# Kernel optimization log

Hardware: AMD Instinct MI355X
Metric: run time of the kernel (lower is better)

The kernel has to match this reference:

```python
import jax, jax.numpy as jnp
import numpy as np

B, N, Q, D, H = 8, 2048, 256, 1024, 16
HD = D // H


def setup_inputs() -> dict:
    key = jax.random.key(0)
    ks = jax.random.split(key, 6)
    scale = 1.0 / np.sqrt(D)
    return {
        "sources": jax.random.normal(ks[0], (B, N, D), dtype=jnp.float32),
        "queries": jax.random.normal(ks[1], (B, Q, D), dtype=jnp.float32),
        "w_in": jax.random.normal(ks[2], (3 * D, D), dtype=jnp.float32) * scale,
        "b_in": jax.random.normal(ks[3], (3 * D,), dtype=jnp.float32) * 0.02,
        "w_out": jax.random.normal(ks[4], (D, D), dtype=jnp.float32) * scale,
        "b_out": jax.random.normal(ks[5], (D,), dtype=jnp.float32) * 0.02,
    }


def reference(sources, queries, w_in, b_in, w_out, b_out):
    # torch nn.MultiheadAttention (batch_first, eval mode, no attn_mask),
    # applied per-sample with equal lengths == one batched cross-attention.
    w_q, w_k, w_v = jnp.split(w_in, 3, axis=0)   # each [D, D]
    b_q, b_k, b_v = jnp.split(b_in, 3, axis=0)
    q = queries @ w_q.T + b_q                    # [B, Q, D]
    k = sources @ w_k.T + b_k                    # [B, N, D]
    v = sources @ w_v.T + b_v                    # [B, N, D]
    q = q.reshape(B, Q, H, HD)
    k = k.reshape(B, N, H, HD)
    v = v.reshape(B, N, H, HD)
    scale = 1.0 / np.sqrt(HD).astype(np.float32)
    scores = jnp.einsum("bqhd,bkhd->bhqk", q, k) * scale  # [B, H, Q, N]
    attn = jax.nn.softmax(scores, axis=-1)
    out = jnp.einsum("bhqk,bkhd->bqhd", attn, v).reshape(B, Q, D)
    out = out @ w_out.T + b_out                  # out_proj
    return out + queries                         # residual (fix=False: no norm)
```

## Files before the change

### kernel.cpp

```cpp
#include <hip/hip_runtime.h>
#include <hip/hip_bf16.h>


typedef unsigned short u16;
typedef __attribute__((ext_vector_type(8))) short short8;
typedef __attribute__((ext_vector_type(4))) float floatx4;

static_assert(sizeof(short8) == 16, "short8 must be 16B");

__device__ __forceinline__ u16 f2bf(float f) {
  unsigned int x = __float_as_uint(f);
  x += 0x7fffu + ((x >> 16) & 1u);
  return (u16)(x >> 16);
}

__device__ __forceinline__ float bf2f(u16 b) {
  return __uint_as_float(((unsigned int)b) << 16);
}

__device__ __forceinline__ void gload16(const u16* g, u16* lds) {
  __builtin_amdgcn_global_load_lds(
      (const __attribute__((address_space(1))) unsigned int*)g,
      (__attribute__((address_space(3))) unsigned int*)lds, 16, 0, 0);
}

template <int N> __device__ __forceinline__ void vmwait() {
  if constexpr (N == 0)      asm volatile("s_waitcnt vmcnt(0)" ::: "memory");
  else if constexpr (N == 4) asm volatile("s_waitcnt vmcnt(4)" ::: "memory");
  else if constexpr (N == 6) asm volatile("s_waitcnt vmcnt(6)" ::: "memory");
  else if constexpr (N == 8) asm volatile("s_waitcnt vmcnt(8)" ::: "memory");
  else static_assert(N == 0, "unsupported vmcnt immediate");
}

__device__ __forceinline__ void lgkm0() {
  asm volatile("s_waitcnt lgkmcnt(0)" ::: "memory");
}

__device__ __forceinline__ void sfence() { __builtin_amdgcn_sched_barrier(0); }

__global__ __launch_bounds__(256) void f2bf_multi(
    const float* __restrict__ s, u16* __restrict__ so,
    const float* __restrict__ q, u16* __restrict__ qo,
    const float* __restrict__ wi, u16* __restrict__ wio,
    const float* __restrict__ wo, u16* __restrict__ woo) {
  int i = blockIdx.x * 256 + threadIdx.x;
  const float* in; u16* out; int idx;
  if (i < 4194304)      { in = s;  out = so;  idx = i; }
  else if (i < 4718592) { in = q;  out = qo;  idx = i - 4194304; }
  else if (i < 5505024) { in = wi; out = wio; idx = i - 4718592; }
  else if (i < 5767168) { in = wo; out = woo; idx = i - 5505024; }
  else return;
  float4 v = reinterpret_cast<const float4*>(in)[idx];
  ushort4 o;
  o.x = f2bf(v.x); o.y = f2bf(v.y); o.z = f2bf(v.z); o.w = f2bf(v.w);
  reinterpret_cast<ushort4*>(out)[idx] = o;
}

template <int MT, int NT>
__device__ __forceinline__ void gemm_core(
    const u16* __restrict__ A, int lda,
    const u16* __restrict__ Bm, int ldb, int K,
    u16* __restrict__ Alds, u16* __restrict__ Blds,
    floatx4 (&acc)[MT][NT]) {
  const int t = threadIdx.x;
  const int wave = t >> 6, lane = t & 63;
  const int rr = lane & 15, kq = lane >> 4;
  constexpr int AI = MT, BI = NT;
  constexpr int AELEMS = MT * 32 * 64;
  constexpr int BELEMS = NT * 32 * 64;

  const u16* ag[AI]; u16* al[AI];
#pragma unroll
  for (int i = 0; i < AI; ++i) {
    int s = i * 256 + t;
    int row = s >> 3, c16 = s & 7;
    ag[i] = A + (size_t)row * lda + ((c16 ^ (row & 7)) * 8);
    al[i] = Alds + (size_t)(i * 256 + wave * 64) * 8;
  }
  const u16* bg[BI]; u16* blp[BI];
#pragma unroll
  for (int i = 0; i < BI; ++i) {
    int s = i * 256 + t;
    int row = s >> 3, c16 = s & 7;
    bg[i] = Bm + (size_t)row * ldb + ((c16 ^ (row & 7)) * 8);
    blp[i] = Blds + (size_t)(i * 256 + wave * 64) * 8;
  }

  const int m0w = (wave & 1) * (MT * 16);
  const int n0w = (wave >> 1) * (NT * 16);
  int aoff[MT][2], boff[NT][2];
#pragma unroll
  for (int mi = 0; mi < MT; ++mi) {
    int row = m0w + mi * 16 + rr;
#pragma unroll
    for (int kk = 0; kk < 2; ++kk)
      aoff[mi][kk] = row * 64 + (((kk * 4 + kq) ^ (row & 7)) * 8);
  }
#pragma unroll
  for (int ni = 0; ni < NT; ++ni) {
    int row = n0w + ni * 16 + rr;
#pragma unroll
    for (int kk = 0; kk < 2; ++kk)
      boff[ni][kk] = row * 64 + (((kk * 4 + kq) ^ (row & 7)) * 8);
  }

  auto compute = [&](int bs) {
    const u16* Ab = Alds + bs * AELEMS;
    const u16* Bb = Blds + bs * BELEMS;
#pragma unroll
    for (int kk = 0; kk < 2; ++kk) {
      short8 af[MT], bfr[NT];
#pragma unroll
      for (int mi = 0; mi < MT; ++mi)
        af[mi] = *reinterpret_cast<const short8*>(Ab + aoff[mi][kk]);
#pragma unroll
      for (int ni = 0; ni < NT; ++ni)
        bfr[ni] = *reinterpret_cast<const short8*>(Bb + boff[ni][kk]);
      __builtin_amdgcn_s_setprio(1);
#pragma unroll
      for (int mi = 0; mi < MT; ++mi)
#pragma unroll
        for (int ni = 0; ni < NT; ++ni)
          acc[mi][ni] = __builtin_amdgcn_mfma_f32_16x16x32_bf16(af[mi], bfr[ni], acc[mi][ni], 0, 0, 0);
      __builtin_amdgcn_s_setprio(0);
    }
  };

  const int nt = K >> 6;

#pragma unroll
  for (int i = 0; i < AI; ++i) gload16(ag[i], al[i]);
#pragma unroll
  for (int i = 0; i < BI; ++i) gload16(bg[i], blp[i]);

  int cur = 0;
#pragma unroll 1
  for (int tt = 0; tt < nt - 1; ++tt) {
    const int nxt = cur ^ 1;
    const int koff = (tt + 1) * 64;
#pragma unroll
    for (int i = 0; i < AI; ++i) gload16(ag[i] + koff, al[i] + nxt * AELEMS);
#pragma unroll
    for (int i = 0; i < BI; ++i) gload16(bg[i] + koff, blp[i] + nxt * BELEMS);
    sfence();
    vmwait<AI + BI>();
    __builtin_amdgcn_s_barrier();
    sfence();
    compute(cur);
    sfence();
    __builtin_amdgcn_s_barrier();
    cur = nxt;
  }
  sfence();
  vmwait<0>();
  __builtin_amdgcn_s_barrier();
  sfence();
  compute(cur);
}

template <int LO>
__device__ __forceinline__ void read_a8(const u16* ab, int kcol0, int kcol1,
                                        short8 (&af)[8][2]) {
#pragma unroll
  for (int mi = 0; mi < 4; ++mi) {
    af[LO + mi][0] = *reinterpret_cast<const short8*>(ab + (LO + mi) * 1024 + kcol0);
    af[LO + mi][1] = *reinterpret_cast<const short8*>(ab + (LO + mi) * 1024 + kcol1);
  }
}

template <int LO>
__device__ __forceinline__ void read_b8(const u16* bb, int kcol0, int kcol1,
                                        short8 (&bf)[4][2]) {
#pragma unroll
  for (int ni = 0; ni < 2; ++ni) {
    bf[LO + ni][0] = *reinterpret_cast<const short8*>(bb + (LO + ni) * 1024 + kcol0);
    bf[LO + ni][1] = *reinterpret_cast<const short8*>(bb + (LO + ni) * 1024 + kcol1);
  }
}

template <int M0, int N0>
__device__ __forceinline__ void quad8(const short8 (&af)[8][2], const short8 (&bf)[4][2],
                                      floatx4 (&acc)[8][4]) {
  __builtin_amdgcn_s_setprio(1);
#pragma unroll
  for (int kk = 0; kk < 2; ++kk)
#pragma unroll
    for (int mi = 0; mi < 4; ++mi)
#pragma unroll
      for (int ni = 0; ni < 2; ++ni)
        acc[M0 + mi][N0 + ni] = __builtin_amdgcn_mfma_f32_16x16x32_bf16(
            af[M0 + mi][kk], bf[N0 + ni][kk], acc[M0 + mi][N0 + ni], 0, 0, 0);
  __builtin_amdgcn_s_setprio(0);
}

__global__ __launch_bounds__(512, 2) void gemm_proj_kv8(
    const u16* __restrict__ s_bf, const u16* __restrict__ wi_bf,
    const float* __restrict__ b_in,
    u16* __restrict__ kp, u16* __restrict__ vT) {
  __shared__ __attribute__((aligned(16))) u16 Alds[2 * 256 * 64];
  __shared__ __attribute__((aligned(16))) u16 Blds[2 * 256 * 64];

  int bid = blockIdx.y * 8 + blockIdx.x;
  int nb = (bid & 7) * 64 + (bid >> 3);
  const int by = nb >> 3, bx = nb & 7;
  const int mB = by * 256;
  const int nB = bx * 256;
  const u16* Ag = s_bf + (size_t)mB * 1024;
  const u16* Wg = wi_bf + (size_t)(1024 + nB) * 1024;
  const float* bias = b_in + 1024 + nB;

  const int t = threadIdx.x;
  const int w = t >> 6, lane = t & 63;
  const int rr = lane & 15, kq = lane >> 4;
  const int wr = w >> 2, wc = w & 3;

  const u16* ga[2][2]; const u16* gb[2][2];
#pragma unroll
  for (int h = 0; h < 2; ++h)
#pragma unroll
    for (int i = 0; i < 2; ++i) {
      int s = i * 512 + t;
      int row = h * 128 + (s >> 3), c16 = s & 7;
      ga[h][i] = Ag + (size_t)row * 1024 + ((c16 ^ (row & 7)) * 8);
      gb[h][i] = Wg + (size_t)row * 1024 + ((c16 ^ (row & 7)) * 8);
    }

#define STAGE_A8(j, h) { const int d_ = ((j) & 1) * 16384;                         \
    gload16(ga[h][0] + (size_t)(j) * 64, Alds + d_ + (h) * 8192 + w * 512);        \
    gload16(ga[h][1] + (size_t)(j) * 64, Alds + d_ + (h) * 8192 + 4096 + w * 512); }
#define STAGE_B8(j, h) { const int d_ = ((j) & 1) * 16384;                         \
    gload16(gb[h][0] + (size_t)(j) * 64, Blds + d_ + (h) * 8192 + w * 512);        \
    gload16(gb[h][1] + (size_t)(j) * 64, Blds + d_ + (h) * 8192 + 4096 + w * 512); }

  const int kcol0 = ((kq) ^ (rr & 7)) * 8;
  const int kcol1 = ((4 + kq) ^ (rr & 7)) * 8;
  const u16* abase = Alds + (wr * 128 + rr) * 64;
  const u16* bbase = Blds + (wc * 64 + rr) * 64;

  short8 af[8][2], bf[4][2];
  const floatx4 zz = {0.f, 0.f, 0.f, 0.f};
  floatx4 acc[8][4];
#pragma unroll
  for (int mi = 0; mi < 8; ++mi)
#pragma unroll
    for (int ni = 0; ni < 4; ++ni) acc[mi][ni] = zz;

  STAGE_A8(0, 0); STAGE_B8(0, 0); STAGE_A8(0, 1); STAGE_B8(0, 1);
  STAGE_A8(1, 0); STAGE_B8(1, 0);
  sfence();
  vmwait<4>();
  __builtin_amdgcn_s_barrier();
  sfence();

#pragma unroll 1
  for (int kt = 0; kt < 16; ++kt) {
    const int doff = (kt & 1) * 16384;
    const u16* ab = abase + doff;
    const u16* bb = bbase + doff;
    read_a8<0>(ab, kcol0, kcol1, af);
    read_b8<0>(bb, kcol0, kcol1, bf);
    if (kt + 1 < 16) STAGE_A8(kt + 1, 1);
    sfence();
    __builtin_amdgcn_s_barrier();
    lgkm0(); sfence();
    quad8<0, 0>(af, bf, acc);
    sfence();
    __builtin_amdgcn_s_barrier();
    sfence();
    read_a8<4>(ab, kcol0, kcol1, af);
    read_b8<2>(bb, kcol0, kcol1, bf);
    if (kt + 1 < 16) STAGE_B8(kt + 1, 1);
    sfence();
    __builtin_amdgcn_s_barrier();
    lgkm0(); sfence();
    quad8<0, 2>(af, bf, acc);
    sfence();
    __builtin_amdgcn_s_barrier();
    sfence();
    if (kt + 2 < 16) STAGE_A8(kt + 2, 0);
    sfence();
    __builtin_amdgcn_s_barrier();
    quad8<4, 0>(af, bf, acc);
    sfence();
    __builtin_amdgcn_s_barrier();
    sfence();
    if (kt + 2 < 16) { STAGE_B8(kt + 2, 0); sfence(); vmwait<4>(); }
    else             { sfence(); vmwait<0>(); }
    __builtin_amdgcn_s_barrier();
    quad8<4, 2>(af, bf, acc);
    sfence();
    __builtin_amdgcn_s_barrier();
    sfence();
  }
#undef STAGE_A8
#undef STAGE_B8

  const int r4 = kq * 4;
  const int m0w = wr * 128, n0w = wc * 64;
  if (nB < 1024) {
#pragma unroll
    for (int mi = 0; mi < 8; ++mi)
#pragma unroll
      for (int ni = 0; ni < 4; ++ni) {
        int nl = n0w + ni * 16 + rr;
        float bv = bias[nl];
#pragma unroll
        for (int r = 0; r < 4; ++r) {
          int m = mB + m0w + mi * 16 + r4 + r;
          kp[(size_t)m * 1024 + nB + nl] = f2bf(acc[mi][ni][r] + bv);
        }
      }
  } else {
#pragma unroll
    for (int mi = 0; mi < 8; ++mi)
#pragma unroll
      for (int ni = 0; ni < 4; ++ni) {
        int n2 = nB + n0w + ni * 16 + rr - 1024;
        int h = n2 >> 6, d = n2 & 63;
        float bv = bias[n0w + ni * 16 + rr];
        int m0 = mB + m0w + mi * 16 + r4;
        int b = m0 >> 11, j0 = m0 & 2047;
        ushort4 o;
        o.x = f2bf(acc[mi][ni][0] + bv);
        o.y = f2bf(acc[mi][ni][1] + bv);
        o.z = f2bf(acc[mi][ni][2] + bv);
        o.w = f2bf(acc[mi][ni][3] + bv);
        *reinterpret_cast<ushort4*>(
            vT + ((size_t)(b * 16 + h) * 64 + d) * 2048 + j0) = o;
      }
  }
}

__global__ __launch_bounds__(256, 2) void gemm_proj_q(
    const u16* __restrict__ qy_bf, const u16* __restrict__ wi_bf,
    const float* __restrict__ b_in, u16* __restrict__ qp) {
  __shared__ __attribute__((aligned(16))) u16 Alds[2 * 128 * 64];
  __shared__ __attribute__((aligned(16))) u16 Blds[2 * 128 * 64];
  const int mB = blockIdx.y * 128;
  const int nB = blockIdx.x * 128;
  const u16* A = qy_bf + (size_t)mB * 1024;
  const u16* W = wi_bf + (size_t)nB * 1024;
  const float* bias = b_in + nB;

  const floatx4 zz = {0.f, 0.f, 0.f, 0.f};
  floatx4 acc[4][4] = {{zz, zz, zz, zz}, {zz, zz, zz, zz}, {zz, zz, zz, zz}, {zz, zz, zz, zz}};
  gemm_core<4, 4>(A, 1024, W, 1024, 1024, Alds, Blds, acc);

  const int lane = threadIdx.x & 63, wave = threadIdx.x >> 6;
  const int rr = lane & 15, r4 = (lane >> 4) * 4;
  const int m0w = (wave & 1) * 64, n0w = (wave >> 1) * 64;
#pragma unroll
  for (int mi = 0; mi < 4; ++mi)
#pragma unroll
    for (int ni = 0; ni < 4; ++ni) {
      int nl = n0w + ni * 16 + rr;
      float bv = bias[nl];
#pragma unroll
      for (int r = 0; r < 4; ++r) {
        int m = mB + m0w + mi * 16 + r4 + r;
        qp[(size_t)m * 1024 + nB + nl] = f2bf((acc[mi][ni][r] + bv) * 0.125f);
      }
    }
}

__global__ __launch_bounds__(512, 2) void attn_fused(
    const u16* __restrict__ qp, const u16* __restrict__ kp,
    const u16* __restrict__ vT, u16* __restrict__ ao) {
  __shared__ __attribute__((aligned(16))) u16 Qlds[8192];
  __shared__ __attribute__((aligned(16))) u16 Klds[2][8192];
  __shared__ __attribute__((aligned(16))) u16 Vlds[2][8192];
  __shared__ __attribute__((aligned(16))) u16 Plds[16384];
  __shared__ float l_part[4][128];

  const int bid = blockIdx.x;
  const int nb = (bid & 7) * 32 + (bid >> 3);
  const int bh = nb >> 1, qh = nb & 1;
  const int b = bh >> 4, h = bh & 15;

  const int t = threadIdx.x;
  const int w = t >> 6, lane = t & 63;
  const int rr = lane & 15, kq = lane >> 4;
  const int swz = rr & 7;
  const int wrS = w >> 2, wcS = w & 3;
  const int wrP = w >> 1, wcP = w & 1;

  const u16* qg[2]; const u16* kg[2]; const u16* vg[2];
  {
    const u16* qbase = qp + ((size_t)(b * 256 + qh * 128)) * 1024 + h * 64;
    const u16* kbase = kp + ((size_t)b * 2048) * 1024 + h * 64;
    const u16* vbase = vT + ((size_t)bh * 64) * 2048;
#pragma unroll
    for (int i = 0; i < 2; ++i) {
      int s = i * 512 + t;
      int r8 = s >> 3, c8 = s & 7;
      int r16 = s >> 4, c16 = s & 15;
      qg[i] = qbase + (size_t)r8 * 1024 + ((c8 ^ (r8 & 7)) * 8);
      kg[i] = kbase + (size_t)r8 * 1024 + ((c8 ^ (r8 & 7)) * 8);
      vg[i] = vbase + (size_t)r16 * 2048 + ((c16 ^ (r16 & 7)) * 8);
    }
  }

  float l_acc[4][4];
#pragma unroll
  for (int mi = 0; mi < 4; ++mi)
#pragma unroll
    for (int r = 0; r < 4; ++r) l_acc[mi][r] = 0.f;
  const floatx4 zz = {0.f, 0.f, 0.f, 0.f};
  floatx4 oacc[2][2] = {{zz, zz}, {zz, zz}};

  ((float*)l_part)[t] = 0.f;
#pragma unroll
  for (int i = 0; i < 2; ++i) gload16(qg[i], Qlds + (i * 512 + w * 64) * 8);
#pragma unroll
  for (int i = 0; i < 2; ++i) gload16(kg[i], &Klds[0][(i * 512 + w * 64) * 8]);
#pragma unroll
  for (int i = 0; i < 2; ++i) gload16(vg[i], &Vlds[0][(i * 512 + w * 64) * 8]);
  sfence();
  vmwait<0>();
  __builtin_amdgcn_s_barrier();
  sfence();

  short8 qf[4][2];
#pragma unroll
  for (int mi = 0; mi < 4; ++mi) {
    int qrow = wrS * 64 + mi * 16 + rr;
#pragma unroll
    for (int kc = 0; kc < 2; ++kc)
      qf[mi][kc] = *reinterpret_cast<const short8*>(
          Qlds + qrow * 64 + (((kc * 4 + kq) ^ swz) * 8));
  }

#pragma unroll 1
  for (int kt = 0; kt < 16; ++kt) {
    const int buf = kt & 1;
    if (kt) { sfence(); __builtin_amdgcn_s_barrier(); sfence(); }
    if (kt < 15) {
      const int nxt = buf ^ 1;
      const size_t ko = (size_t)(kt + 1) * 131072;
      const size_t vo = (size_t)(kt + 1) * 128;
#pragma unroll
      for (int i = 0; i < 2; ++i) gload16(kg[i] + ko, &Klds[nxt][(i * 512 + w * 64) * 8]);
#pragma unroll
      for (int i = 0; i < 2; ++i) gload16(vg[i] + vo, &Vlds[nxt][(i * 512 + w * 64) * 8]);
      sfence();
      vmwait<4>();
    } else {
      sfence();
      vmwait<0>();
    }
    short8 kf[2][2];
#pragma unroll
    for (int ni = 0; ni < 2; ++ni) {
      int krow = wcS * 32 + ni * 16 + rr;
#pragma unroll
      for (int kc = 0; kc < 2; ++kc)
        kf[ni][kc] = *reinterpret_cast<const short8*>(
            &Klds[buf][krow * 64 + (((kc * 4 + kq) ^ swz) * 8)]);
    }
    lgkm0(); sfence();
    floatx4 sacc[4][2];
#pragma unroll
    for (int mi = 0; mi < 4; ++mi)
#pragma unroll
      for (int ni = 0; ni < 2; ++ni) sacc[mi][ni] = zz;
    __builtin_amdgcn_s_setprio(1);
#pragma unroll
    for (int kc = 0; kc < 2; ++kc)
#pragma unroll
      for (int mi = 0; mi < 4; ++mi)
#pragma unroll
        for (int ni = 0; ni < 2; ++ni)
          sacc[mi][ni] = __builtin_amdgcn_mfma_f32_16x16x32_bf16(
              qf[mi][kc], kf[ni][kc], sacc[mi][ni], 0, 0, 0);
    __builtin_amdgcn_s_setprio(0);
    sfence();
#pragma unroll
    for (int mi = 0; mi < 4; ++mi) {
#pragma unroll
      for (int r = 0; r < 4; ++r) {
        int qr = wrS * 64 + mi * 16 + kq * 4 + r;
        int rb = qr * 128;
        int qsw = qr & 7;
        float lsum = 0.f;
#pragma unroll
        for (int ni = 0; ni < 2; ++ni) {
          int key = wcS * 32 + ni * 16 + rr;
          u16 pb = f2bf(__expf(sacc[mi][ni][r]));
          Plds[rb + ((((key >> 3) ^ qsw)) << 3) + (key & 7)] = pb;
          lsum += bf2f(pb);
        }
        l_acc[mi][r] += lsum;
      }
    }
    lgkm0();
    sfence();
    __builtin_amdgcn_s_barrier();
    sfence();
    short8 pa[2][4], vf[2][4];
#pragma unroll
    for (int mi = 0; mi < 2; ++mi) {
      int qrow = wrP * 32 + mi * 16 + rr;
#pragma unroll
      for (int kc = 0; kc < 4; ++kc)
        pa[mi][kc] = *reinterpret_cast<const short8*>(
            Plds + qrow * 128 + ((((kc * 4 + kq) ^ swz)) << 3));
    }
#pragma unroll
    for (int ni = 0; ni < 2; ++ni) {
      int drow = wcP * 32 + ni * 16 + rr;
#pragma unroll
      for (int kc = 0; kc < 4; ++kc)
        vf[ni][kc] = *reinterpret_cast<const short8*>(
            &Vlds[buf][drow * 128 + ((((kc * 4 + kq) ^ swz)) << 3)]);
    }
    lgkm0(); sfence();
    __builtin_amdgcn_s_setprio(1);
#pragma unroll
    for (int kc = 0; kc < 4; ++kc)
#pragma unroll
      for (int mi = 0; mi < 2; ++mi)
#pragma unroll
        for (int ni = 0; ni < 2; ++ni)
          oacc[mi][ni] = __builtin_amdgcn_mfma_f32_16x16x32_bf16(
              pa[mi][kc], vf[ni][kc], oacc[mi][ni], 0, 0, 0);
    __builtin_amdgcn_s_setprio(0);
    sfence();
  }

#pragma unroll
  for (int mi = 0; mi < 4; ++mi)
#pragma unroll
    for (int r = 0; r < 4; ++r) {
      float v = l_acc[mi][r];
      v += __shfl_xor(v, 1, 64);
      v += __shfl_xor(v, 2, 64);
      v += __shfl_xor(v, 4, 64);
      v += __shfl_xor(v, 8, 64);
      l_acc[mi][r] = v;
    }
  if (rr == 0) {
#pragma unroll
    for (int mi = 0; mi < 4; ++mi)
#pragma unroll
      for (int r = 0; r < 4; ++r)
        l_part[wcS][wrS * 64 + mi * 16 + kq * 4 + r] = l_acc[mi][r];
  }
  __syncthreads();

  u16* aob = ao + ((size_t)(b * 256 + qh * 128)) * 1024 + h * 64;
#pragma unroll
  for (int mi = 0; mi < 2; ++mi)
#pragma unroll
    for (int r = 0; r < 4; ++r) {
      int q = wrP * 32 + mi * 16 + kq * 4 + r;
      float inv = 1.0f / (l_part[0][q] + l_part[1][q] + l_part[2][q] + l_part[3][q]);
#pragma unroll
      for (int ni = 0; ni < 2; ++ni) {
        int d = wcP * 32 + ni * 16 + rr;
        aob[(size_t)q * 1024 + d] = f2bf(oacc[mi][ni][r] * inv);
      }
    }
}

__global__ __launch_bounds__(256, 2) void gemm_out(
    const u16* __restrict__ A, const u16* __restrict__ W,
    const float* __restrict__ bias, const float* __restrict__ resid,
    float* __restrict__ out) {
  __shared__ __attribute__((aligned(16))) u16 Alds[2 * 64 * 64];
  __shared__ __attribute__((aligned(16))) u16 Blds[2 * 128 * 64];
  const int mB = blockIdx.y * 64;
  const int nB = blockIdx.x * 128;
  const floatx4 zz = {0.f, 0.f, 0.f, 0.f};
  floatx4 acc[2][4] = {{zz, zz, zz, zz}, {zz, zz, zz, zz}};
  gemm_core<2, 4>(A + (size_t)mB * 1024, 1024, W + (size_t)nB * 1024, 1024, 1024,
                  Alds, Blds, acc);
  const int lane = threadIdx.x & 63, wave = threadIdx.x >> 6;
  const int rr = lane & 15, r4 = (lane >> 4) * 4;
  const int m0w = (wave & 1) * 32, n0w = (wave >> 1) * 64;
#pragma unroll
  for (int mi = 0; mi < 2; ++mi)
#pragma unroll
    for (int ni = 0; ni < 4; ++ni) {
      int n = nB + n0w + ni * 16 + rr;
      float bv = bias[n];
#pragma unroll
      for (int r = 0; r < 4; ++r) {
        int m = mB + m0w + mi * 16 + r4 + r;
        size_t idx = (size_t)m * 1024 + n;
        out[idx] = acc[mi][ni][r] + bv + resid[idx];
      }
    }
}

extern "C" void kernel_launch(void* const* d_in, const int* in_sizes, int n_in,
                              void* d_out, int out_size, void* d_ws, size_t ws_size,
                              hipStream_t stream) {
  const float* sources = (const float*)d_in[0];
  const float* queries = (const float*)d_in[1];
  const float* w_in    = (const float*)d_in[2];
  const float* b_in    = (const float*)d_in[3];
  const float* w_out   = (const float*)d_in[4];
  const float* b_out   = (const float*)d_in[5];
  float* out = (float*)d_out;

  char* ws = (char*)d_ws;
  size_t off = 0;
  auto alloc = [&](size_t elems) -> u16* {
    u16* p = (u16*)(ws + off);
    off += elems * sizeof(u16);
    off = (off + 255) & ~(size_t)255;
    return p;
  };
  u16* s_bf  = alloc((size_t)16777216);
  u16* qy_bf = alloc((size_t)2097152);
  u16* wi_bf = alloc((size_t)3145728);
  u16* wo_bf = alloc((size_t)1048576);
  u16* qp    = alloc((size_t)2097152);
  u16* kp    = alloc((size_t)16777216);
  u16* vT    = alloc((size_t)16777216);
  u16* ao    = alloc((size_t)2097152);

  f2bf_multi<<<dim3(22528), 256, 0, stream>>>(
      sources, s_bf, queries, qy_bf, w_in, wi_bf, w_out, wo_bf);

  gemm_proj_kv8<<<dim3(8, 64), 512, 0, stream>>>(s_bf, wi_bf, b_in, kp, vT);
  gemm_proj_q<<<dim3(8, 16), 256, 0, stream>>>(qy_bf, wi_bf, b_in, qp);

  attn_fused<<<dim3(256), 512, 0, stream>>>(qp, kp, vT, ao);

  gemm_out<<<dim3(8, 32), 256, 0, stream>>>(ao, wo_bf, b_out, queries, out);
}
```

Measured before the change: 275.8 us.

## Restructure attention kernel into 64-query blocks with MFMA row-sum and staggered K/V prefetch

```diff
diff --git a/kernel.cpp b/kernel.cpp
--- a/kernel.cpp
+++ b/kernel.cpp
@@ -14,8 +14,10 @@
   return (u16)(x >> 16);
 }
 
-__device__ __forceinline__ float bf2f(u16 b) {
-  return __uint_as_float(((unsigned int)b) << 16);
+__device__ __forceinline__ unsigned int cvtpk(float lo, float hi) {
+  unsigned int r;
+  asm("v_cvt_pk_bf16_f32 %0, %1, %2" : "=v"(r) : "v"(lo), "v"(hi));
+  return r;
 }
 
 __device__ __forceinline__ void gload16(const u16* g, u16* lds) {
@@ -26,6 +28,7 @@
 
 template <int N> __device__ __forceinline__ void vmwait() {
   if constexpr (N == 0)      asm volatile("s_waitcnt vmcnt(0)" ::: "memory");
+  else if constexpr (N == 2) asm volatile("s_waitcnt vmcnt(2)" ::: "memory");
   else if constexpr (N == 4) asm volatile("s_waitcnt vmcnt(4)" ::: "memory");
   else if constexpr (N == 6) asm volatile("s_waitcnt vmcnt(6)" ::: "memory");
   else if constexpr (N == 8) asm volatile("s_waitcnt vmcnt(8)" ::: "memory");
@@ -363,202 +366,178 @@
     }
 }
 
-__global__ __launch_bounds__(512, 2) void attn_fused(
+__global__ __launch_bounds__(512, 4) void attn_fused(
     const u16* __restrict__ qp, const u16* __restrict__ kp,
     const u16* __restrict__ vT, u16* __restrict__ ao) {
-  __shared__ __attribute__((aligned(16))) u16 Qlds[8192];
   __shared__ __attribute__((aligned(16))) u16 Klds[2][8192];
   __shared__ __attribute__((aligned(16))) u16 Vlds[2][8192];
-  __shared__ __attribute__((aligned(16))) u16 Plds[16384];
-  __shared__ float l_part[4][128];
+  __shared__ __attribute__((aligned(16))) u16 Plds[8192];
 
   const int bid = blockIdx.x;
-  const int nb = (bid & 7) * 32 + (bid >> 3);
-  const int bh = nb >> 1, qh = nb & 1;
+  const int nb = (bid & 7) * 64 + (bid >> 3);
+  const int bh = nb >> 2, qb = nb & 3;
   const int b = bh >> 4, h = bh & 15;
 
   const int t = threadIdx.x;
   const int w = t >> 6, lane = t & 63;
   const int rr = lane & 15, kq = lane >> 4;
-  const int swz = rr & 7;
-  const int wrS = w >> 2, wcS = w & 3;
-  const int wrP = w >> 1, wcP = w & 1;
-
-  const u16* qg[2]; const u16* kg[2]; const u16* vg[2];
+  const int wk = w >> 1, wq = w & 1;
+  const int wPq = w >> 2, wPd = w & 3;
+
+  const u16* qg;
+  const u16* kg[2];
+  const u16* vg[2];
   {
-    const u16* qbase = qp + ((size_t)(b * 256 + qh * 128)) * 1024 + h * 64;
+    const u16* qbase = qp + ((size_t)(b * 256 + qb * 64)) * 1024 + h * 64;
     const u16* kbase = kp + ((size_t)b * 2048) * 1024 + h * 64;
     const u16* vbase = vT + ((size_t)bh * 64) * 2048;
+    { int row = t >> 3, c8 = t & 7;
+      qg = qbase + (size_t)row * 1024 + ((c8 ^ (row & 7)) * 8); }
 #pragma unroll
     for (int i = 0; i < 2; ++i) {
       int s = i * 512 + t;
       int r8 = s >> 3, c8 = s & 7;
       int r16 = s >> 4, c16 = s & 15;
-      qg[i] = qbase + (size_t)r8 * 1024 + ((c8 ^ (r8 & 7)) * 8);
       kg[i] = kbase + (size_t)r8 * 1024 + ((c8 ^ (r8 & 7)) * 8);
       vg[i] = vbase + (size_t)r16 * 2048 + ((c16 ^ (r16 & 7)) * 8);
     }
   }
 
-  float l_acc[4][4];
-#pragma unroll
-  for (int mi = 0; mi < 4; ++mi)
-#pragma unroll
-    for (int r = 0; r < 4; ++r) l_acc[mi][r] = 0.f;
-  const floatx4 zz = {0.f, 0.f, 0.f, 0.f};
-  floatx4 oacc[2][2] = {{zz, zz}, {zz, zz}};
-
-  ((float*)l_part)[t] = 0.f;
-#pragma unroll
-  for (int i = 0; i < 2; ++i) gload16(qg[i], Qlds + (i * 512 + w * 64) * 8);
-#pragma unroll
-  for (int i = 0; i < 2; ++i) gload16(kg[i], &Klds[0][(i * 512 + w * 64) * 8]);
-#pragma unroll
-  for (int i = 0; i < 2; ++i) gload16(vg[i], &Vlds[0][(i * 512 + w * 64) * 8]);
+#define STAGE_K(j) { u16* d_ = &Klds[(j) & 1][w * 512];                 \
+    gload16(kg[0] + (size_t)(j) * 131072, d_);                          \
+    gload16(kg[1] + (size_t)(j) * 131072, d_ + 4096); }
+#define STAGE_V(j) { u16* d_ = &Vlds[(j) & 1][w * 512];                 \
+    gload16(vg[0] + (size_t)(j) * 128, d_);                             \
+    gload16(vg[1] + (size_t)(j) * 128, d_ + 4096); }
+
+  gload16(qg, Plds + w * 512);
+  STAGE_K(0); STAGE_V(0); STAGE_K(1);
   sfence();
-  vmwait<0>();
+  vmwait<6>();
   __builtin_amdgcn_s_barrier();
   sfence();
-
-  short8 qf[4][2];
-#pragma unroll
-  for (int mi = 0; mi < 4; ++mi) {
-    int qrow = wrS * 64 + mi * 16 + rr;
+  short8 qf[2][2];
+#pragma unroll
+  for (int ni = 0; ni < 2; ++ni) {
+    int qrow = wq * 32 + ni * 16 + rr;
 #pragma unroll
     for (int kc = 0; kc < 2; ++kc)
-      qf[mi][kc] = *reinterpret_cast<const short8*>(
-          Qlds + qrow * 64 + (((kc * 4 + kq) ^ swz) * 8));
-  }
+      qf[ni][kc] = *reinterpret_cast<const short8*>(
+          Plds + qrow * 64 + (((kc * 4 + kq) ^ (qrow & 7)) * 8));
+  }
+  lgkm0(); sfence();
+  vmwait<2>();
+  __builtin_amdgcn_s_barrier();
+  sfence();
+
+  const short ov = (rr == 0) ? (short)0x3F80 : (short)0;
+  const short8 ones = {ov, ov, ov, ov, ov, ov, ov, ov};
+  const floatx4 zz = {0.f, 0.f, 0.f, 0.f};
+  floatx4 oacc[2] = {zz, zz};
+  floatx4 acc_l[2] = {zz, zz};
+
+  const int pq0 = wq * 32 + rr;
+  const int pkb = wk * 4 + (kq >> 1);
+  const int pk4 = (kq & 1) * 4;
 
 #pragma unroll 1
   for (int kt = 0; kt < 16; ++kt) {
     const int buf = kt & 1;
-    if (kt) { sfence(); __builtin_amdgcn_s_barrier(); sfence(); }
-    if (kt < 15) {
-      const int nxt = buf ^ 1;
-      const size_t ko = (size_t)(kt + 1) * 131072;
-      const size_t vo = (size_t)(kt + 1) * 128;
-#pragma unroll
-      for (int i = 0; i < 2; ++i) gload16(kg[i] + ko, &Klds[nxt][(i * 512 + w * 64) * 8]);
-#pragma unroll
-      for (int i = 0; i < 2; ++i) gload16(vg[i] + vo, &Vlds[nxt][(i * 512 + w * 64) * 8]);
-      sfence();
-      vmwait<4>();
-    } else {
-      sfence();
-      vmwait<0>();
-    }
+    if (kt + 1 < 16) STAGE_V(kt + 1);
+    sfence();
     short8 kf[2][2];
 #pragma unroll
-    for (int ni = 0; ni < 2; ++ni) {
-      int krow = wcS * 32 + ni * 16 + rr;
+    for (int mi = 0; mi < 2; ++mi) {
+      int krow = wk * 32 + mi * 16 + rr;
 #pragma unroll
       for (int kc = 0; kc < 2; ++kc)
-        kf[ni][kc] = *reinterpret_cast<const short8*>(
-            &Klds[buf][krow * 64 + (((kc * 4 + kq) ^ swz) * 8)]);
+        kf[mi][kc] = *reinterpret_cast<const short8*>(
+            &Klds[buf][krow * 64 + (((kc * 4 + kq) ^ (krow & 7)) * 8)]);
     }
     lgkm0(); sfence();
-    floatx4 sacc[4][2];
-#pragma unroll
-    for (int mi = 0; mi < 4; ++mi)
-#pragma unroll
-      for (int ni = 0; ni < 2; ++ni) sacc[mi][ni] = zz;
+    floatx4 sacc[2][2] = {{zz, zz}, {zz, zz}};
     __builtin_amdgcn_s_setprio(1);
 #pragma unroll
     for (int kc = 0; kc < 2; ++kc)
 #pragma unroll
-      for (int mi = 0; mi < 4; ++mi)
+      for (int mi = 0; mi < 2; ++mi)
 #pragma unroll
         for (int ni = 0; ni < 2; ++ni)
           sacc[mi][ni] = __builtin_amdgcn_mfma_f32_16x16x32_bf16(
-              qf[mi][kc], kf[ni][kc], sacc[mi][ni], 0, 0, 0);
+              kf[mi][kc], qf[ni][kc], sacc[mi][ni], 0, 0, 0);
     __builtin_amdgcn_s_setprio(0);
     sfence();
 #pragma unroll
-    for (int mi = 0; mi < 4; ++mi) {
-#pragma unroll
-      for (int r = 0; r < 4; ++r) {
-        int qr = wrS * 64 + mi * 16 + kq * 4 + r;
-        int rb = qr * 128;
-        int qsw = qr & 7;
-        float lsum = 0.f;
-#pragma unroll
-        for (int ni = 0; ni < 2; ++ni) {
-          int key = wcS * 32 + ni * 16 + rr;
-          u16 pb = f2bf(__expf(sacc[mi][ni][r]));
-          Plds[rb + ((((key >> 3) ^ qsw)) << 3) + (key & 7)] = pb;
-          lsum += bf2f(pb);
-        }
-        l_acc[mi][r] += lsum;
+    for (int mi = 0; mi < 2; ++mi) {
+      int kb = pkb + mi * 2;
+#pragma unroll
+      for (int ni = 0; ni < 2; ++ni) {
+        int q = pq0 + ni * 16;
+        float e0 = __expf(sacc[mi][ni][0]);
+        float e1 = __expf(sacc[mi][ni][1]);
+        float e2 = __expf(sacc[mi][ni][2]);
+        float e3 = __expf(sacc[mi][ni][3]);
+        uint2 pv;
+        pv.x = cvtpk(e0, e1);
+        pv.y = cvtpk(e2, e3);
+        *reinterpret_cast<uint2*>(
+            &Plds[q * 128 + ((kb ^ (q & 7)) << 3) + pk4]) = pv;
       }
     }
-    lgkm0();
-    sfence();
-    __builtin_amdgcn_s_barrier();
-    sfence();
-    short8 pa[2][4], vf[2][4];
+    lgkm0(); sfence();
+    if (kt < 15) vmwait<4>(); else vmwait<0>();
+    __builtin_amdgcn_s_barrier();
+    sfence();
+    short8 pa[2][4], vf[4];
 #pragma unroll
     for (int mi = 0; mi < 2; ++mi) {
-      int qrow = wrP * 32 + mi * 16 + rr;
+      int qrow = wPq * 32 + mi * 16 + rr;
 #pragma unroll
       for (int kc = 0; kc < 4; ++kc)
         pa[mi][kc] = *reinterpret_cast<const short8*>(
-            Plds + qrow * 128 + ((((kc * 4 + kq) ^ swz)) << 3));
-    }
-#pragma unroll
-    for (int ni = 0; ni < 2; ++ni) {
-      int drow = wcP * 32 + ni * 16 + rr;
+            Plds + qrow * 128 + (((kc * 4 + kq) ^ (qrow & 7)) << 3));
+    }
+    {
+      int drow = wPd * 16 + rr;
 #pragma unroll
       for (int kc = 0; kc < 4; ++kc)
-        vf[ni][kc] = *reinterpret_cast<const short8*>(
-            &Vlds[buf][drow * 128 + ((((kc * 4 + kq) ^ swz)) << 3)]);
+        vf[kc] = *reinterpret_cast<const short8*>(
+            &Vlds[buf][drow * 128 + (((kc * 4 + kq) ^ (drow & 7)) << 3)]);
     }
     lgkm0(); sfence();
+    if (kt + 2 < 16) STAGE_K(kt + 2);
+    sfence();
     __builtin_amdgcn_s_setprio(1);
 #pragma unroll
     for (int kc = 0; kc < 4; ++kc)
 #pragma unroll
-      for (int mi = 0; mi < 2; ++mi)
-#pragma unroll
-        for (int ni = 0; ni < 2; ++ni)
-          oacc[mi][ni] = __builtin_amdgcn_mfma_f32_16x16x32_bf16(
-              pa[mi][kc], vf[ni][kc], oacc[mi][ni], 0, 0, 0);
+      for (int mi = 0; mi < 2; ++mi) {
+        oacc[mi] = __builtin_amdgcn_mfma_f32_16x16x32_bf16(
+            pa[mi][kc], vf[kc], oacc[mi], 0, 0, 0);
+        acc_l[mi] = __builtin_amdgcn_mfma_f32_16x16x32_bf16(
+            pa[mi][kc], ones, acc_l[mi], 0, 0, 0);
+      }
     __builtin_amdgcn_s_setprio(0);
     sfence();
-  }
-
-#pragma unroll
-  for (int mi = 0; mi < 4; ++mi)
+    if (kt + 1 < 16) {
+      if (kt + 2 < 16) vmwait<4>(); else vmwait<2>();
+    }
+    __builtin_amdgcn_s_barrier();
+    sfence();
+  }
+#undef STAGE_K
+#undef STAGE_V
+
+  u16* aob = ao + ((size_t)(b * 256 + qb * 64)) * 1024 + h * 64;
+#pragma unroll
+  for (int mi = 0; mi < 2; ++mi)
 #pragma unroll
     for (int r = 0; r < 4; ++r) {
-      float v = l_acc[mi][r];
-      v += __shfl_xor(v, 1, 64);
-      v += __shfl_xor(v, 2, 64);
-      v += __shfl_xor(v, 4, 64);
-      v += __shfl_xor(v, 8, 64);
-      l_acc[mi][r] = v;
-    }
-  if (rr == 0) {
-#pragma unroll
-    for (int mi = 0; mi < 4; ++mi)
-#pragma unroll
-      for (int r = 0; r < 4; ++r)
-        l_part[wcS][wrS * 64 + mi * 16 + kq * 4 + r] = l_acc[mi][r];
-  }
-  __syncthreads();
-
-  u16* aob = ao + ((size_t)(b * 256 + qh * 128)) * 1024 + h * 64;
-#pragma unroll
-  for (int mi = 0; mi < 2; ++mi)
-#pragma unroll
-    for (int r = 0; r < 4; ++r) {
-      int q = wrP * 32 + mi * 16 + kq * 4 + r;
-      float inv = 1.0f / (l_part[0][q] + l_part[1][q] + l_part[2][q] + l_part[3][q]);
-#pragma unroll
-      for (int ni = 0; ni < 2; ++ni) {
-        int d = wcP * 32 + ni * 16 + rr;
-        aob[(size_t)q * 1024 + d] = f2bf(oacc[mi][ni][r] * inv);
-      }
+      float l = __shfl(acc_l[mi][r], lane & 48, 64);
+      float inv = 1.0f / l;
+      int q = wPq * 32 + mi * 16 + kq * 4 + r;
+      int d = wPd * 16 + rr;
+      aob[(size_t)q * 1024 + d] = f2bf(oacc[mi][r] * inv);
     }
 }
 
@@ -626,7 +605,7 @@
   gemm_proj_kv8<<<dim3(8, 64), 512, 0, stream>>>(s_bf, wi_bf, b_in, kp, vT);
   gemm_proj_q<<<dim3(8, 16), 256, 0, stream>>>(qy_bf, wi_bf, b_in, qp);
 
-  attn_fused<<<dim3(256), 512, 0, stream>>>(qp, kp, vT, ao);
+  attn_fused<<<dim3(512), 512, 0, stream>>>(qp, kp, vT, ao);
 
   gemm_out<<<dim3(8, 32), 256, 0, stream>>>(ao, wo_bf, b_out, queries, out);
 }
```

Measured after the change: 267.6 us. 3.0% less time.
